# Optimization experiments

Hardware: AMD Instinct MI355X
Metric: run time of the kernel (lower is better)

Reference implementation:

```python
import jax, jax.numpy as jnp
import numpy as np

N = 50000   # nodes
E = 800000  # edges
IN, H, OUT = 64, 512, 128


def _lin_init(key, out_dim, in_dim):
    kw, kb = jax.random.split(key)
    bound = 1.0 / np.sqrt(in_dim)
    W = jax.random.uniform(kw, (out_dim, in_dim), jnp.float32, -bound, bound)
    b = jax.random.uniform(kb, (out_dim,), jnp.float32, -bound, bound)
    return W, b


def setup_inputs() -> dict:
    key = jax.random.key(0)
    ks = jax.random.split(key, 10)
    x = jax.random.normal(ks[0], (N, IN), jnp.float32)
    edge_index = jax.random.randint(ks[1], (2, E), 0, N, jnp.int64)
    W_s1, b_s1 = _lin_init(ks[2], H, IN)
    W_s2, b_s2 = _lin_init(ks[3], H, H)
    W_s3, b_s3 = _lin_init(ks[4], H, H)
    W_s4, b_s4 = _lin_init(ks[5], H, H)
    W_m1, b_m1 = _lin_init(ks[6], OUT, H)
    W_m2, b_m2 = _lin_init(ks[7], OUT, OUT)
    W_l1, b_l1 = _lin_init(ks[8], OUT, H)
    W_l2, b_l2 = _lin_init(ks[9], OUT, OUT)
    return {"x": x, "edge_index": edge_index,
            "W_s1": W_s1, "b_s1": b_s1, "W_s2": W_s2, "b_s2": b_s2,
            "W_s3": W_s3, "b_s3": b_s3, "W_s4": W_s4, "b_s4": b_s4,
            "W_m1": W_m1, "b_m1": b_m1, "W_m2": W_m2, "b_m2": b_m2,
            "W_l1": W_l1, "b_l1": b_l1, "W_l2": W_l2, "b_l2": b_l2}


def _aggregate(h, src, dst):
    # GINConv with default eps=0: (1+eps)*x + sum_{j in N(i)} x_j
    return h + jax.ops.segment_sum(h[src], dst, num_segments=N)


def reference(x, edge_index,
              W_s1, b_s1, W_s2, b_s2, W_s3, b_s3, W_s4, b_s4,
              W_m1, b_m1, W_m2, b_m2, W_l1, b_l1, W_l2, b_l2):
    src, dst = edge_index[0], edge_index[1]
    lrelu = lambda v: jax.nn.leaky_relu(v, 0.1)

    def mlp_shared(h):
        h = lrelu(h @ W_s1.T + b_s1)
        h = lrelu(h @ W_s2.T + b_s2)
        h = lrelu(h @ W_s3.T + b_s3)
        return h @ W_s4.T + b_s4

    def mlp_mu(h):
        return jax.nn.relu(h @ W_m1.T + b_m1) @ W_m2.T + b_m2

    def mlp_logvar(h):
        return jax.nn.relu(h @ W_l1.T + b_l1) @ W_l2.T + b_l2

    h = jax.nn.relu(mlp_shared(_aggregate(x, src, dst)))
    mu = mlp_mu(_aggregate(h, src, dst))
    logvar = mlp_logvar(_aggregate(h, src, dst))
    return (mu, logvar)
```

## Files before the change

### kernel.cpp

```cpp
#include <hip/hip_runtime.h>
#include <hip/hip_bf16.h>
#include <stdint.h>

#define N_NODES 50000
#define N_PAD   50048
#define E_EDGES 800000
#define MT      391

typedef __bf16 bf16x8 __attribute__((ext_vector_type(8)));
typedef __bf16 bf16x4 __attribute__((ext_vector_type(4)));
typedef float  f32x4  __attribute__((ext_vector_type(4)));

__global__ void count_deg(const int* __restrict__ ei, int* __restrict__ cnt) {
    int e = blockIdx.x * blockDim.x + threadIdx.x;
    if (e < E_EDGES) atomicAdd(&cnt[ei[E_EDGES + e]], 1);
}

#define SCAN_B 1024
__global__ void scan_block(const int* __restrict__ cnt, int* __restrict__ ptr,
                           int* __restrict__ bsum, int n) {
    __shared__ int buf[SCAN_B];
    int i = blockIdx.x * SCAN_B + threadIdx.x;
    int v = (i < n) ? cnt[i] : 0;
    buf[threadIdx.x] = v;
    __syncthreads();
    #pragma unroll
    for (int off = 1; off < SCAN_B; off <<= 1) {
        int t = (threadIdx.x >= (unsigned)off) ? buf[threadIdx.x - off] : 0;
        __syncthreads();
        buf[threadIdx.x] += t;
        __syncthreads();
    }
    if (i < n) ptr[i] = buf[threadIdx.x] - v;
    if (threadIdx.x == SCAN_B - 1) bsum[blockIdx.x] = buf[SCAN_B - 1];
}

__global__ void scan_bsums(const int* __restrict__ bsum, int* __restrict__ boff,
                           int nb, int* __restrict__ total_out) {
    __shared__ int buf[SCAN_B];
    int v = ((int)threadIdx.x < nb) ? bsum[threadIdx.x] : 0;
    buf[threadIdx.x] = v;
    __syncthreads();
    #pragma unroll
    for (int off = 1; off < SCAN_B; off <<= 1) {
        int t = (threadIdx.x >= (unsigned)off) ? buf[threadIdx.x - off] : 0;
        __syncthreads();
        buf[threadIdx.x] += t;
        __syncthreads();
    }
    if ((int)threadIdx.x < nb) boff[threadIdx.x] = buf[threadIdx.x] - v;
    if (threadIdx.x == SCAN_B - 1) *total_out = buf[SCAN_B - 1];
}

__global__ void scan_add(int* __restrict__ ptr, const int* __restrict__ boff, int n) {
    int i = blockIdx.x * SCAN_B + threadIdx.x;
    if (i < n) ptr[i] += boff[blockIdx.x];
}

__global__ void fill_csr(const int* __restrict__ ei, const int* __restrict__ ptr,
                         int* __restrict__ cursor, int* __restrict__ col) {
    int e = blockIdx.x * blockDim.x + threadIdx.x;
    if (e < E_EDGES) {
        int dst = ei[E_EDGES + e];
        int pos = ptr[dst] + atomicAdd(&cursor[dst], 1);
        col[pos] = ei[e];
    }
}

#define XN      3200000
#define WTOT    983040
__global__ void cvt_all(const float* __restrict__ x,
                        const float* __restrict__ Ws1, const float* __restrict__ Ws2,
                        const float* __restrict__ Ws3, const float* __restrict__ Ws4,
                        const float* __restrict__ Wm1, const float* __restrict__ Wl1,
                        const float* __restrict__ Wm2, const float* __restrict__ Wl2,
                        __bf16* __restrict__ xb, __bf16* __restrict__ wbuf) {
    int i = blockIdx.x * blockDim.x + threadIdx.x;
    if (i < XN) { xb[i] = (__bf16)x[i]; return; }
    int j = i - XN;
    if (j >= WTOT) return;
    const float* s; int o;
    if      (j <  32768) { s = Ws1; o = j; }
    else if (j < 294912) { s = Ws2; o = j -  32768; }
    else if (j < 557056) { s = Ws3; o = j - 294912; }
    else if (j < 819200) { s = Ws4; o = j - 557056; }
    else if (j < 884736) { s = Wm1; o = j - 819200; }
    else if (j < 950272) { s = Wl1; o = j - 884736; }
    else if (j < 966656) { s = Wm2; o = j - 950272; }
    else                 { s = Wl2; o = j - 966656; }
    wbuf[j] = (__bf16)s[o];
}

__global__ __launch_bounds__(256) void agg0_gather(
    const __bf16* __restrict__ xb, const int* __restrict__ ptr,
    const int* __restrict__ col, __bf16* __restrict__ out) {
    int node = blockIdx.x * 4 + (threadIdx.x >> 6);
    int lane = threadIdx.x & 63;
    int g    = lane >> 3;
    int f0   = (lane & 7) << 3;
    if (node >= N_PAD) return;
    long o = (long)node * 64 + f0;
    if (node >= N_NODES) {
        if (g == 0) {
            bf16x8 z;
            #pragma unroll
            for (int i = 0; i < 8; ++i) z[i] = (__bf16)0.0f;
            *(bf16x8*)&out[o] = z;
        }
        return;
    }
    float a[8];
    #pragma unroll
    for (int i = 0; i < 8; ++i) a[i] = 0.0f;
    if (g == 0) {
        bf16x8 s = *(const bf16x8*)&xb[o];
        #pragma unroll
        for (int i = 0; i < 8; ++i) a[i] = (float)s[i];
    }
    int e0 = ptr[node], e1 = ptr[node + 1];
    int e = e0;
    for (; e + 16 <= e1; e += 16) {
        int c0 = col[e + g];
        int c1 = col[e + 8 + g];
        bf16x8 v0 = *(const bf16x8*)&xb[(c0 << 6) + f0];
        bf16x8 v1 = *(const bf16x8*)&xb[(c1 << 6) + f0];
        #pragma unroll
        for (int i = 0; i < 8; ++i) a[i] += (float)v0[i] + (float)v1[i];
    }
    int rem = e1 - e;
    if (rem > 0) {
        int u0 = (g < rem) ? g : 0;        float m0 = (g < rem) ? 1.0f : 0.0f;
        int i1 = g + 8;
        int u1 = (i1 < rem) ? i1 : 0;      float m1 = (i1 < rem) ? 1.0f : 0.0f;
        int c0 = col[e + u0];
        int c1 = col[e + u1];
        bf16x8 v0 = *(const bf16x8*)&xb[(c0 << 6) + f0];
        bf16x8 v1 = *(const bf16x8*)&xb[(c1 << 6) + f0];
        #pragma unroll
        for (int i = 0; i < 8; ++i) a[i] += m0 * (float)v0[i] + m1 * (float)v1[i];
    }
    #pragma unroll
    for (int i = 0; i < 8; ++i) {
        a[i] += __shfl_xor(a[i], 8, 64);
        a[i] += __shfl_xor(a[i], 16, 64);
        a[i] += __shfl_xor(a[i], 32, 64);
    }
    if (g == 0) {
        bf16x8 r;
        #pragma unroll
        for (int i = 0; i < 8; ++i) r[i] = (__bf16)a[i];
        *(bf16x8*)&out[o] = r;
    }
}

__global__ __launch_bounds__(256) void aggt_gather(
    const __bf16* __restrict__ t, const int* __restrict__ ptr,
    const int* __restrict__ col, const float* __restrict__ b_m1,
    const float* __restrict__ b_l1, __bf16* __restrict__ p) {
    int node = blockIdx.x * 8 + (threadIdx.x >> 5);
    if (node >= N_NODES) return;
    int hl = threadIdx.x & 31;
    int f0 = hl << 3;
    float a[8];
    {
        bf16x8 s = *(const bf16x8*)&t[((long)node << 8) + f0];
        #pragma unroll
        for (int i = 0; i < 8; ++i) a[i] = (float)s[i];
    }
    int e0 = ptr[node], e1 = ptr[node + 1];
    int e = e0;
    for (; e + 8 <= e1; e += 8) {
        int c[8];
        #pragma unroll
        for (int u = 0; u < 8; ++u) c[u] = col[e + u];
        bf16x8 v[8];
        #pragma unroll
        for (int u = 0; u < 8; ++u) v[u] = *(const bf16x8*)&t[((long)c[u] << 8) + f0];
        #pragma unroll
        for (int u = 0; u < 8; ++u)
            #pragma unroll
            for (int i = 0; i < 8; ++i) a[i] += (float)v[u][i];
    }
    int rem = e1 - e;
    if (rem > 0) {
        #pragma unroll
        for (int u = 0; u < 7; ++u) {
            int   uu = (u < rem) ? u : 0;
            float m  = (u < rem) ? 1.0f : 0.0f;
            int   cc = col[e + uu];
            bf16x8 v = *(const bf16x8*)&t[((long)cc << 8) + f0];
            #pragma unroll
            for (int i = 0; i < 8; ++i) a[i] += m * (float)v[i];
        }
    }
    const float* bp = (f0 < 128) ? (b_m1 + f0) : (b_l1 + (f0 - 128));
    f32x4 b0 = *(const f32x4*)bp;
    f32x4 b1 = *(const f32x4*)(bp + 4);
    bf16x8 r;
    #pragma unroll
    for (int i = 0; i < 4; ++i) r[i]     = (__bf16)fmaxf(a[i]     + b0[i], 0.0f);
    #pragma unroll
    for (int i = 0; i < 4; ++i) r[4 + i] = (__bf16)fmaxf(a[4 + i] + b1[i], 0.0f);
    *(bf16x8*)&p[((long)node << 8) + f0] = r;
}

__device__ __forceinline__ void gl_lds16(const __bf16* g, __bf16* l) {
    __builtin_amdgcn_global_load_lds(
        (const __attribute__((address_space(1))) uint32_t*)g,
        (__attribute__((address_space(3))) uint32_t*)l, 16, 0, 0);
}

template <int NCOL>
__device__ __forceinline__ void swizzle_xy(int bid, int& x, int& y) {
    int grp  = bid / (8 * NCOL);
    int rem  = bid - grp * (8 * NCOL);
    int base = grp * 8;
    int width = MT - base; if (width > 8) width = 8;
    x = base + rem % width;
    y = rem / width;
}

template <int ACT, bool BIAS, bool OUT_BF16, bool MCHK>
__device__ __forceinline__ void gemm_core(
    const __bf16* __restrict__ A, int lda, const __bf16* __restrict__ W,
    const float* __restrict__ bias, void* __restrict__ Cout, int ldc,
    int K, long Mstore, long blockRow, int blockCol,
    __bf16* __restrict__ smem) {
    __bf16* As = smem;
    __bf16* Ws = smem + 8192;
    const int tid  = threadIdx.x;
    const int wid  = tid >> 6;
    const int lane = tid & 63;
    const int wm = (wid >> 1) << 6;
    const int wn = (wid & 1) << 6;

    f32x4 acc[4][4];
    #pragma unroll
    for (int i = 0; i < 4; ++i)
        #pragma unroll
        for (int j = 0; j < 4; ++j) acc[i][j] = (f32x4)0.0f;

    const int srow = lane >> 3;
    const int skg  = (lane & 7) ^ srow;
    const __bf16* gA[4]; const __bf16* gW[4];
    __bf16 *lA[4], *lW[4];
    #pragma unroll
    for (int i = 0; i < 4; ++i) {
        int c = wid * 4 + i;
        gA[i] = A + (blockRow + c * 8 + srow) * (long)lda + skg * 8;
        gW[i] = W + ((long)blockCol + c * 8 + srow) * (long)K + skg * 8;
        lA[i] = As + c * 512;
        lW[i] = Ws + c * 512;
    }

    const int rA = lane & 15;
    const int q  = lane >> 4;
    const int r7 = rA & 7;

    for (int k0 = 0; k0 < K; k0 += 64) {
        #pragma unroll
        for (int i = 0; i < 4; ++i) gl_lds16(gA[i] + k0, lA[i]);
        #pragma unroll
        for (int i = 0; i < 4; ++i) gl_lds16(gW[i] + k0, lW[i]);
        __syncthreads();

        #pragma unroll
        for (int s = 0; s < 2; ++s) {
            const int slot = ((s * 4 + q) ^ r7) * 8;
            bf16x8 af[4], bf[4];
            #pragma unroll
            for (int mi = 0; mi < 4; ++mi)
                af[mi] = *(const bf16x8*)&As[(wm + mi * 16 + rA) * 64 + slot];
            #pragma unroll
            for (int ni = 0; ni < 4; ++ni)
                bf[ni] = *(const bf16x8*)&Ws[(wn + ni * 16 + rA) * 64 + slot];
            #pragma unroll
            for (int mi = 0; mi < 4; ++mi)
                #pragma unroll
                for (int ni = 0; ni < 4; ++ni)
                    acc[mi][ni] = __builtin_amdgcn_mfma_f32_16x16x32_bf16(
                        af[mi], bf[ni], acc[mi][ni], 0, 0, 0);
        }
        __syncthreads();
    }

    const int ccol = lane & 15;
    const int crow = (lane >> 4) << 2;
    if (OUT_BF16 && !MCHK) {
        #pragma unroll
        for (int mi = 0; mi < 4; ++mi) {
            #pragma unroll
            for (int ni = 0; ni < 4; ++ni) {
                int gc = wn + ni * 16 + ccol;
                float bv = BIAS ? bias[blockCol + gc] : 0.0f;
                #pragma unroll
                for (int r = 0; r < 4; ++r) {
                    float v = acc[mi][ni][r] + bv;
                    if (ACT == 1) v = (v > 0.0f) ? v : 0.1f * v;
                    else if (ACT == 2) v = fmaxf(v, 0.0f);
                    smem[(wm + mi * 16 + crow + r) * 128 + gc] = (__bf16)v;
                }
            }
        }
        __syncthreads();
        #pragma unroll
        for (int i = 0; i < 8; ++i) {
            int o   = (i * 256 + tid) * 8;
            int row = o >> 7;
            int co  = o & 127;
            *(bf16x8*)((__bf16*)Cout + (blockRow + row) * (long)ldc + blockCol + co) =
                *(const bf16x8*)&smem[o];
        }
    } else if (!OUT_BF16) {
        float* fsmem = (float*)smem;
        #pragma unroll
        for (int half = 0; half < 2; ++half) {
            __syncthreads();
            if ((wm >> 6) == half) {
                #pragma unroll
                for (int mi = 0; mi < 4; ++mi) {
                    #pragma unroll
                    for (int ni = 0; ni < 4; ++ni) {
                        int gc = wn + ni * 16 + ccol;
                        float bv = BIAS ? bias[blockCol + gc] : 0.0f;
                        #pragma unroll
                        for (int r = 0; r < 4; ++r) {
                            float v = acc[mi][ni][r] + bv;
                            if (ACT == 1) v = (v > 0.0f) ? v : 0.1f * v;
                            else if (ACT == 2) v = fmaxf(v, 0.0f);
                            fsmem[(mi * 16 + crow + r) * 128 + gc] = v;
                        }
                    }
                }
            }
            __syncthreads();
            #pragma unroll
            for (int i = 0; i < 8; ++i) {
                int o   = i * 256 + tid;
                int row = o >> 5;
                int co  = (o & 31) * 4;
                long gr = blockRow + half * 64 + row;
                if (!MCHK || gr < Mstore)
                    *(f32x4*)((float*)Cout + gr * (long)ldc + blockCol + co) =
                        *(const f32x4*)&fsmem[o * 4];
            }
        }
    } else {
        #pragma unroll
        for (int mi = 0; mi < 4; ++mi) {
            #pragma unroll
            for (int ni = 0; ni < 4; ++ni) {
                long gr0 = blockRow + wm + mi * 16 + crow;
                int  gc  = blockCol + wn + ni * 16 + ccol;
                float bv = BIAS ? bias[gc] : 0.0f;
                #pragma unroll
                for (int r = 0; r < 4; ++r) {
                    long gr = gr0 + r;
                    if (!MCHK || gr < Mstore) {
                        float v = acc[mi][ni][r] + bv;
                        if (ACT == 1) v = (v > 0.0f) ? v : 0.1f * v;
                        else if (ACT == 2) v = fmaxf(v, 0.0f);
                        ((__bf16*)Cout)[gr * ldc + gc] = (__bf16)v;
                    }
                }
            }
        }
    }
}

template <int NCOL, int ACT, bool BIAS, bool OUT_BF16, bool MCHK>
__global__ __launch_bounds__(256) void gemm_bt(
    const __bf16* __restrict__ A, int lda, const __bf16* __restrict__ W,
    const float* __restrict__ bias, void* __restrict__ Cout, int ldc,
    int K, long Mstore) {
    __shared__ __bf16 smem[128 * 128];
    int x, y;
    swizzle_xy<NCOL>(blockIdx.x, x, y);
    gemm_core<ACT, BIAS, OUT_BF16, MCHK>(A, lda, W, bias, Cout, ldc, K, Mstore,
                                         (long)x * 128, y * 128, smem);
}

__global__ __launch_bounds__(256) void gemm_heads(
    const __bf16* __restrict__ p, const __bf16* __restrict__ wm2,
    const float* __restrict__ b_m2, float* __restrict__ mu,
    const __bf16* __restrict__ wl2, const float* __restrict__ b_l2,
    float* __restrict__ lv) {
    __shared__ __bf16 smem[128 * 128];
    int x, hd;
    swizzle_xy<2>(blockIdx.x, x, hd);
    if (hd == 0)
        gemm_core<0, true, false, true>(p, 256, wm2, b_m2, mu, 128, 128, N_NODES,
                                        (long)x * 128, 0, smem);
    else
        gemm_core<0, true, false, true>(p + 128, 256, wl2, b_l2, lv, 128, 128, N_NODES,
                                        (long)x * 128, 0, smem);
}

extern "C" void kernel_launch(void* const* d_in, const int* in_sizes, int n_in,
                              void* d_out, int out_size, void* d_ws, size_t ws_size,
                              hipStream_t stream) {
    const float* x    = (const float*)d_in[0];
    const int*   ei   = (const int*)d_in[1];
    const float* W_s1 = (const float*)d_in[2];
    const float* b_s1 = (const float*)d_in[3];
    const float* W_s2 = (const float*)d_in[4];
    const float* b_s2 = (const float*)d_in[5];
    const float* W_s3 = (const float*)d_in[6];
    const float* b_s3 = (const float*)d_in[7];
    const float* W_s4 = (const float*)d_in[8];
    const float* b_s4 = (const float*)d_in[9];
    const float* W_m1 = (const float*)d_in[10];
    const float* b_m1 = (const float*)d_in[11];
    const float* W_m2 = (const float*)d_in[12];
    const float* b_m2 = (const float*)d_in[13];
    const float* W_l1 = (const float*)d_in[14];
    const float* b_l1 = (const float*)d_in[15];
    const float* W_l2 = (const float*)d_in[16];
    const float* b_l2 = (const float*)d_in[17];

    char* ws = (char*)d_ws;
    size_t off = 0;
    auto carve = [&](size_t bytes) -> void* {
        void* p = ws + off;
        off = (off + bytes + 255) & ~(size_t)255;
        return p;
    };
    int* ptr  = (int*)carve((size_t)(N_NODES + 1) * 4);
    int* col  = (int*)carve((size_t)E_EDGES * 4);
    int* bsum = (int*)carve(SCAN_B * 4);
    int* boff = (int*)carve(SCAN_B * 4);
    __bf16* wbuf = (__bf16*)carve((size_t)WTOT * 2);
    __bf16* w1  = wbuf;
    __bf16* w2  = wbuf +  32768;
    __bf16* w3  = wbuf + 294912;
    __bf16* w4  = wbuf + 557056;
    __bf16* wml = wbuf + 819200;
    __bf16* wm2 = wbuf + 950272;
    __bf16* wl2 = wbuf + 966656;
    __bf16* xb    = (__bf16*)carve((size_t)XN * 2);
    __bf16* agg0b = (__bf16*)carve((size_t)N_PAD * 64 * 2);
    __bf16* B1    = (__bf16*)carve((size_t)N_PAD * 512 * 2);
    __bf16* B2    = (__bf16*)carve((size_t)N_PAD * 512 * 2);

    int* cnt = (int*)B1;
    int* cur = (int*)B2;

    (void)hipMemsetAsync(cnt, 0, (size_t)N_NODES * 4, stream);
    (void)hipMemsetAsync(cur, 0, (size_t)N_NODES * 4, stream);

    const int NB = (N_NODES + SCAN_B - 1) / SCAN_B;
    count_deg<<<E_EDGES / 256, 256, 0, stream>>>(ei, cnt);
    scan_block<<<NB, SCAN_B, 0, stream>>>(cnt, ptr, bsum, N_NODES);
    scan_bsums<<<1, SCAN_B, 0, stream>>>(bsum, boff, NB, &ptr[N_NODES]);
    scan_add<<<NB, SCAN_B, 0, stream>>>(ptr, boff, N_NODES);
    fill_csr<<<E_EDGES / 256, 256, 0, stream>>>(ei, ptr, cur, col);

    cvt_all<<<(XN + WTOT + 255) / 256, 256, 0, stream>>>(
        x, W_s1, W_s2, W_s3, W_s4, W_m1, W_l1, W_m2, W_l2, xb, wbuf);

    agg0_gather<<<N_PAD / 4, 256, 0, stream>>>(xb, ptr, col, agg0b);

    gemm_bt<4, 1, true, true, false><<<MT * 4, 256, 0, stream>>>(agg0b, 64, w1, b_s1, B1, 512, 64, N_PAD);
    gemm_bt<4, 1, true, true, false><<<MT * 4, 256, 0, stream>>>(B1, 512, w2, b_s2, B2, 512, 512, N_PAD);
    gemm_bt<4, 1, true, true, false><<<MT * 4, 256, 0, stream>>>(B2, 512, w3, b_s3, B1, 512, 512, N_PAD);
    gemm_bt<4, 2, true, true, false><<<MT * 4, 256, 0, stream>>>(B1, 512, w4, b_s4, B2, 512, 512, N_PAD);

    __bf16* t = B1;
    gemm_bt<2, 0, false, true, false><<<MT * 2, 256, 0, stream>>>(B2, 512, wml, nullptr, t, 256, 512, N_PAD);

    __bf16* p = B2;
    aggt_gather<<<(N_NODES + 7) / 8, 256, 0, stream>>>(t, ptr, col, b_m1, b_l1, p);

    float* mu = (float*)d_out;
    float* lv = mu + (size_t)N_NODES * 128;
    gemm_heads<<<MT * 2, 256, 0, stream>>>(p, wm2, b_m2, mu, wl2, b_l2, lv);
}
```

Baseline: 485.1 us.

## Fuse shared MLP and projection GEMMs into one LDS-resident kernel

Replaces five separate GEMM launches (four shared-MLP layers plus the mu/logvar projection) with a single kernel that keeps a 64-row activation tile in LDS across all layers. Weights are streamed through double-buffered LDS chunks via global_load_lds, and the next layer's first chunk is prefetched during the current layer's last chunk. This removes the intermediate 50k×512 bf16 activation round-trips through global memory and the launch overhead. In exchange, each block re-streams every weight matrix for only 64 rows. It also uses about 136KB of LDS per block, which limits occupancy to one block per CU.

```diff
diff --git a/kernel.cpp b/kernel.cpp
--- a/kernel.cpp
+++ b/kernel.cpp
@@ -210,6 +210,199 @@
         (__attribute__((address_space(3))) uint32_t*)l, 16, 0, 0);
 }
 
+__device__ __forceinline__ void stage_w(const __bf16* __restrict__ W, int K, int k0,
+                                        __bf16* __restrict__ buf, int nrows,
+                                        int wid, int lane) {
+    int ipw = nrows >> 7;
+    int r16 = lane >> 2, sl = lane & 3;
+    #pragma unroll
+    for (int i = 0; i < 4; ++i) {
+        if (i < ipw) {
+            int cc = wid * ipw + i;
+            int r  = cc * 16 + r16;
+            int kt = sl ^ ((r >> 1) & 3);
+            gl_lds16(W + (long)r * K + k0 + kt * 8, buf + cc * 512);
+        }
+    }
+}
+
+template <int NI>
+__device__ __forceinline__ void chunk_mfma(const __bf16* __restrict__ sAct,
+    const __bf16* __restrict__ buf, int c, int rA, int q, int wncol,
+    f32x4 (&acc)[4][NI]) {
+    const int g   = c * 4 + q;
+    const int sla = ((g & 56) | ((g & 7) ^ (rA & 7))) << 3;
+    bf16x8 af[4], bfr[NI];
+    #pragma unroll
+    for (int mi = 0; mi < 4; ++mi)
+        af[mi] = *(const bf16x8*)&sAct[(mi * 16 + rA) * 512 + sla];
+    #pragma unroll
+    for (int ni = 0; ni < NI; ++ni) {
+        int wr = wncol + ni * 16 + rA;
+        bfr[ni] = *(const bf16x8*)&buf[wr * 32 + ((q ^ ((wr >> 1) & 3)) << 3)];
+    }
+    #pragma unroll
+    for (int mi = 0; mi < 4; ++mi)
+        #pragma unroll
+        for (int ni = 0; ni < NI; ++ni)
+            acc[mi][ni] = __builtin_amdgcn_mfma_f32_16x16x32_bf16(
+                af[mi], bfr[ni], acc[mi][ni], 0, 0, 0);
+}
+
+__device__ __forceinline__ void chunk_mfma_a0(const __bf16* __restrict__ act0,
+    const __bf16* __restrict__ buf, int c, int rA, int q, int wncol,
+    f32x4 (&acc)[4][4]) {
+    const int g   = c * 4 + q;
+    const int sla = (g ^ (rA & 7)) << 3;
+    bf16x8 af[4], bfr[4];
+    #pragma unroll
+    for (int mi = 0; mi < 4; ++mi)
+        af[mi] = *(const bf16x8*)&act0[(mi * 16 + rA) * 64 + sla];
+    #pragma unroll
+    for (int ni = 0; ni < 4; ++ni) {
+        int wr = wncol + ni * 16 + rA;
+        bfr[ni] = *(const bf16x8*)&buf[wr * 32 + ((q ^ ((wr >> 1) & 3)) << 3)];
+    }
+    #pragma unroll
+    for (int mi = 0; mi < 4; ++mi)
+        #pragma unroll
+        for (int ni = 0; ni < 4; ++ni)
+            acc[mi][ni] = __builtin_amdgcn_mfma_f32_16x16x32_bf16(
+                af[mi], bfr[ni], acc[mi][ni], 0, 0, 0);
+}
+
+template <int ACTn>
+__device__ __forceinline__ void writeback_act(__bf16* __restrict__ sAct,
+    f32x4 (&acc)[4][4], const float* __restrict__ bias,
+    int wn, int ccol, int crow) {
+    float bv[4];
+    #pragma unroll
+    for (int ni = 0; ni < 4; ++ni) bv[ni] = bias[wn + ni * 16 + ccol];
+    #pragma unroll
+    for (int mi = 0; mi < 4; ++mi)
+        #pragma unroll
+        for (int ni = 0; ni < 4; ++ni) {
+            int cc = wn + ni * 16 + ccol;
+            int g  = cc >> 3;
+            #pragma unroll
+            for (int p = 0; p < 4; ++p) {
+                int rr = mi * 16 + crow + p;
+                float v = acc[mi][ni][p] + bv[ni];
+                if (ACTn == 1) v = (v > 0.0f) ? v : 0.1f * v;
+                else           v = fmaxf(v, 0.0f);
+                int sl = (g & 56) | ((g & 7) ^ (rr & 7));
+                sAct[rr * 512 + sl * 8 + (cc & 7)] = (__bf16)v;
+            }
+        }
+}
+
+template <int ACTn>
+__device__ __forceinline__ void layer512(__bf16* __restrict__ sAct,
+    __bf16* __restrict__ bufA, __bf16* __restrict__ bufB,
+    const __bf16* __restrict__ W, const __bf16* __restrict__ Wnext,
+    int nrows_next, const float* __restrict__ bias,
+    int wn, int rA, int q, int ccol, int crow, int wid, int lane) {
+    f32x4 acc[4][4];
+    #pragma unroll
+    for (int i = 0; i < 4; ++i)
+        #pragma unroll
+        for (int j = 0; j < 4; ++j) acc[i][j] = (f32x4)0.0f;
+    #pragma unroll
+    for (int c = 0; c < 16; ++c) {
+        if (c < 15) stage_w(W, 512, (c + 1) * 32, (c & 1) ? bufA : bufB, 512, wid, lane);
+        else        stage_w(Wnext, 512, 0, bufA, nrows_next, wid, lane);
+        chunk_mfma<4>(sAct, (c & 1) ? bufB : bufA, c, rA, q, wn, acc);
+        __syncthreads();
+    }
+    writeback_act<ACTn>(sAct, acc, bias, wn, ccol, crow);
+    __syncthreads();
+}
+
+__global__ __launch_bounds__(512) void mlp_fused(
+    const __bf16* __restrict__ a0,
+    const __bf16* __restrict__ w1, const float* __restrict__ b1,
+    const __bf16* __restrict__ w2, const float* __restrict__ b2,
+    const __bf16* __restrict__ w3, const float* __restrict__ b3,
+    const __bf16* __restrict__ w4, const float* __restrict__ b4,
+    const __bf16* __restrict__ wp,
+    __bf16* __restrict__ tg)
+{
+    __shared__ __bf16 lds[69632];
+    __bf16* act0 = lds;
+    __bf16* sAct = lds + 4096;
+    __bf16* bufA = lds + 36864;
+    __bf16* bufB = lds + 53248;
+
+    const int tid  = threadIdx.x;
+    const int wid  = tid >> 6;
+    const int lane = tid & 63;
+    const long blockRow = (long)blockIdx.x * 64;
+
+    const int rA   = lane & 15;
+    const int q    = lane >> 4;
+    const int ccol = lane & 15;
+    const int crow = (lane >> 4) << 2;
+    const int wn   = wid << 6;
+    const int wnp  = wid << 5;
+
+    {
+        int srow = lane >> 3;
+        int skg  = (lane & 7) ^ srow;
+        gl_lds16(a0 + (blockRow + wid * 8 + srow) * 64 + skg * 8, act0 + wid * 512);
+    }
+    stage_w(w1, 64, 0, bufA, 512, wid, lane);
+    __syncthreads();
+
+    {
+        f32x4 acc[4][4];
+        #pragma unroll
+        for (int i = 0; i < 4; ++i)
+            #pragma unroll
+            for (int j = 0; j < 4; ++j) acc[i][j] = (f32x4)0.0f;
+        stage_w(w1, 64, 32, bufB, 512, wid, lane);
+        chunk_mfma_a0(act0, bufA, 0, rA, q, wn, acc);
+        __syncthreads();
+        stage_w(w2, 512, 0, bufA, 512, wid, lane);
+        chunk_mfma_a0(act0, bufB, 1, rA, q, wn, acc);
+        __syncthreads();
+        writeback_act<1>(sAct, acc, b1, wn, ccol, crow);
+        __syncthreads();
+    }
+
+    layer512<1>(sAct, bufA, bufB, w2, w3, 512, b2, wn, rA, q, ccol, crow, wid, lane);
+    layer512<1>(sAct, bufA, bufB, w3, w4, 512, b3, wn, rA, q, ccol, crow, wid, lane);
+    layer512<2>(sAct, bufA, bufB, w4, wp, 256, b4, wn, rA, q, ccol, crow, wid, lane);
+
+    {
+        f32x4 accp[4][2];
+        #pragma unroll
+        for (int i = 0; i < 4; ++i)
+            #pragma unroll
+            for (int j = 0; j < 2; ++j) accp[i][j] = (f32x4)0.0f;
+        #pragma unroll
+        for (int c = 0; c < 16; ++c) {
+            if (c < 15) stage_w(wp, 512, (c + 1) * 32, (c & 1) ? bufA : bufB, 256, wid, lane);
+            chunk_mfma<2>(sAct, (c & 1) ? bufB : bufA, c, rA, q, wnp, accp);
+            __syncthreads();
+        }
+        #pragma unroll
+        for (int mi = 0; mi < 4; ++mi)
+            #pragma unroll
+            for (int ni = 0; ni < 2; ++ni)
+                #pragma unroll
+                for (int p = 0; p < 4; ++p)
+                    bufA[(mi * 16 + crow + p) * 256 + wnp + ni * 16 + ccol] =
+                        (__bf16)accp[mi][ni][p];
+        __syncthreads();
+        int rr = tid >> 3;
+        int c0 = (tid & 7) << 5;
+        const bf16x8* s = (const bf16x8*)&bufA[rr * 256 + c0];
+        __bf16* d = tg + (blockRow + rr) * 256 + c0;
+        #pragma unroll
+        for (int i = 0; i < 4; ++i) *(bf16x8*)(d + i * 8) = s[i];
+    }
+}
+
 template <int NCOL>
 __device__ __forceinline__ void swizzle_xy(int bid, int& x, int& y) {
     int grp  = bid / (8 * NCOL);
@@ -366,18 +559,6 @@
             }
         }
     }
-}
-
-template <int NCOL, int ACT, bool BIAS, bool OUT_BF16, bool MCHK>
-__global__ __launch_bounds__(256) void gemm_bt(
-    const __bf16* __restrict__ A, int lda, const __bf16* __restrict__ W,
-    const float* __restrict__ bias, void* __restrict__ Cout, int ldc,
-    int K, long Mstore) {
-    __shared__ __bf16 smem[128 * 128];
-    int x, y;
-    swizzle_xy<NCOL>(blockIdx.x, x, y);
-    gemm_core<ACT, BIAS, OUT_BF16, MCHK>(A, lda, W, bias, Cout, ldc, K, Mstore,
-                                         (long)x * 128, y * 128, smem);
 }
 
 __global__ __launch_bounds__(256) void gemm_heads(
@@ -460,13 +641,9 @@
 
     agg0_gather<<<N_PAD / 4, 256, 0, stream>>>(xb, ptr, col, agg0b);
 
-    gemm_bt<4, 1, true, true, false><<<MT * 4, 256, 0, stream>>>(agg0b, 64, w1, b_s1, B1, 512, 64, N_PAD);
-    gemm_bt<4, 1, true, true, false><<<MT * 4, 256, 0, stream>>>(B1, 512, w2, b_s2, B2, 512, 512, N_PAD);
-    gemm_bt<4, 1, true, true, false><<<MT * 4, 256, 0, stream>>>(B2, 512, w3, b_s3, B1, 512, 512, N_PAD);
-    gemm_bt<4, 2, true, true, false><<<MT * 4, 256, 0, stream>>>(B1, 512, w4, b_s4, B2, 512, 512, N_PAD);
-
     __bf16* t = B1;
-    gemm_bt<2, 0, false, true, false><<<MT * 2, 256, 0, stream>>>(B2, 512, wml, nullptr, t, 256, 512, N_PAD);
+    mlp_fused<<<N_PAD / 64, 512, 0, stream>>>(agg0b, w1, b_s1, w2, b_s2,
+                                              w3, b_s3, w4, b_s4, wml, t);
 
     __bf16* p = B2;
     aggt_gather<<<(N_NODES + 7) / 8, 256, 0, stream>>>(t, ptr, col, b_m1, b_l1, p);
```

Result: faster. 465.1 us (-4.1%).
